# Optimization experiments

Hardware: AMD Instinct MI355X
Metric: run time of the kernel (lower is better)

## Reference

```python
import jax, jax.numpy as jnp
import numpy as np

N = 4096          # number of agents
TOP_K = 12        # config.TOP_K
OBS_RADIUS = 1.0  # config.OBS_RADIUS


def setup_inputs() -> dict:
    key = jax.random.key(0)
    ks = jax.random.split(key, 10)

    def lin(k, o, i):
        return jax.random.normal(k, (o, i), dtype=jnp.float32) * (1.0 / np.sqrt(i))

    x = jax.random.normal(ks[0], (N, N, 4), dtype=jnp.float32)
    r = jnp.asarray(0.25, dtype=jnp.float32)  # safety radius subtracted from d_norm
    W1 = lin(ks[1], 64, 6);   b1 = jax.random.normal(ks[2], (64,), jnp.float32) * 0.01
    W2 = lin(ks[3], 128, 64); b2 = jax.random.normal(ks[4], (128,), jnp.float32) * 0.01
    W3 = lin(ks[5], 64, 128); b3 = jax.random.normal(ks[6], (64,), jnp.float32) * 0.01
    W4 = lin(ks[7], 1, 64);   b4 = jax.random.normal(ks[8], (1,), jnp.float32) * 0.01
    return {"x": x, "r": r, "W1": W1, "b1": b1, "W2": W2, "b2": b2,
            "W3": W3, "b3": b3, "W4": W4, "b4": b4}


def reference(x, r, W1, b1, W2, b2, W3, b3, W4, b4):
    n = x.shape[0]
    # d_norm with eps added INSIDE the sum (matches torch: sum(x**2 + 1e-4))
    d_norm = jnp.sqrt(jnp.sum(x[:, :, :2] ** 2 + 0.0001, axis=2, keepdims=True))  # [n,n,1]
    eye = jnp.eye(n, dtype=x.dtype)[:, :, None]                                   # [n,n,1]
    xf = jnp.concatenate([x, eye, d_norm - r], axis=2)                            # [n,n,6]

    # remove_distant_agents: top-k nearest by 2D norm (eps 1e-6 inside sum)
    dn = jnp.sqrt(jnp.sum(xf[:, :, :2] ** 2 + 1e-06, axis=2))                     # [n,n]
    _, idx = jax.lax.top_k(-dn, TOP_K)                                            # [n,K]
    xg = jnp.take_along_axis(xf, idx[:, :, None], axis=1)                         # [n,K,6]

    dist = jnp.sqrt(jnp.sum(xg[:, :, :2] ** 2 + 0.0001, axis=2, keepdims=True))   # [n,K,1]
    mask = (dist <= OBS_RADIUS).astype(xg.dtype)

    # 1x1 Conv1d stack == per-neighbor MLP
    h = jax.nn.relu(jnp.einsum('nkc,oc->nko', xg, W1) + b1)
    h = jax.nn.relu(jnp.einsum('nkc,oc->nko', h, W2) + b2)
    h = jax.nn.relu(jnp.einsum('nkc,oc->nko', h, W3) + b3)
    out = (jnp.einsum('nkc,oc->nko', h, W4) + b4) * mask                          # [n,K,1]

    rows = jnp.broadcast_to(jnp.arange(n)[:, None], (n, TOP_K))
    indices = jnp.stack([rows, idx], axis=2).reshape(-1, 2)                       # [n*K,2]
    return out, mask, indices
```

## Files before the change

kernel.cpp:

```cpp
#include <hip/hip_runtime.h>

#define NN    4096
#define TOPK  12
#define NP    (NN * TOPK)
#define OFF_MASK (NP)
#define OFF_IDX  (2 * NP)

__global__ __launch_bounds__(256) void topk_rows(const float* __restrict__ x,
                                                 float* __restrict__ out) {
    const int i = blockIdx.x;
    const int t = threadIdx.x;
    const float4* x4 = (const float4*)x + (size_t)i * NN;

    float s[16];
    #pragma unroll
    for (int k = 0; k < 16; ++k) {
        float4 v = x4[(k << 8) + t];
        s[k] = v.x * v.x + v.y * v.y;
    }

    float bs = s[0];
    int   bj = t;
    #pragma unroll
    for (int k = 1; k < 16; ++k) {
        int j = (k << 8) + t;
        if (s[k] < bs) { bs = s[k]; bj = j; }
    }

    __shared__ float red_s[4];
    __shared__ int   red_j[4];
    __shared__ int   sel[TOPK];

    for (int it = 0; it < TOPK; ++it) {
        float vs = bs;
        int   vj = bj;
        #pragma unroll
        for (int off = 1; off < 64; off <<= 1) {
            float os = __shfl_xor(vs, off, 64);
            int   oj = __shfl_xor(vj, off, 64);
            if (os < vs || (os == vs && oj < vj)) { vs = os; vj = oj; }
        }
        int wid = t >> 6;
        if ((t & 63) == 0) { red_s[wid] = vs; red_j[wid] = vj; }
        __syncthreads();
        float ms = red_s[0];
        int   mj = red_j[0];
        #pragma unroll
        for (int w = 1; w < 4; ++w) {
            float osw = red_s[w]; int ojw = red_j[w];
            if (osw < ms || (osw == ms && ojw < mj)) { ms = osw; mj = ojw; }
        }
        if (t == 0) sel[it] = mj;
        if ((mj & 255) == t) {
            int kk = mj >> 8;
            #pragma unroll
            for (int k = 0; k < 16; ++k)
                if (k == kk) s[k] = 3.0e38f;
            bs = s[0]; bj = t;
            #pragma unroll
            for (int k = 1; k < 16; ++k) {
                int j = (k << 8) + t;
                if (s[k] < bs) { bs = s[k]; bj = j; }
            }
        }
        __syncthreads();
    }

    if (t < TOPK) {
        int j = sel[t];
        float4 v = x4[j];
        float ss = v.x * v.x + v.y * v.y;
        float d  = sqrtf(ss + 2.0e-4f);
        float mask = (d <= 1.0f) ? 1.0f : 0.0f;
        int p = i * TOPK + t;
        out[OFF_MASK + p]        = mask;
        out[OFF_IDX + 2 * p]     = (float)i;
        out[OFF_IDX + 2 * p + 1] = (float)j;
    }
}

__global__ __launch_bounds__(512, 6) void mlp_block(
        const float* __restrict__ x, const float* __restrict__ rp,
        const float* __restrict__ W1, const float* __restrict__ b1,
        const float* __restrict__ W2, const float* __restrict__ b2,
        const float* __restrict__ W3, const float* __restrict__ b3,
        const float* __restrict__ W4, const float* __restrict__ b4,
        float* out) {
    __shared__ float h1s[64 * 64];
    __shared__ float h2s[128 * 64];
    __shared__ float p4s[8 * 64];

    const int t  = threadIdx.x;
    const int pl = t & 63;
    const int ch = __builtin_amdgcn_readfirstlane(t >> 6);
    const int p  = blockIdx.x * 64 + pl;
    const int i  = p / TOPK;
    const int j  = (int)out[OFF_IDX + 2 * p + 1];

    const float4 v = ((const float4*)x)[(size_t)i * NN + j];
    const float d  = sqrtf(v.x * v.x + v.y * v.y + 2.0e-4f);
    float xin[6];
    xin[0] = v.x; xin[1] = v.y; xin[2] = v.z; xin[3] = v.w;
    xin[4] = (i == j) ? 1.0f : 0.0f;
    xin[5] = d - rp[0];

    #pragma unroll
    for (int q = 0; q < 8; ++q) {
        int m = ch * 8 + q;
        const float* w = W1 + m * 6;
        float a = b1[m];
        #pragma unroll
        for (int c = 0; c < 6; ++c) a += w[c] * xin[c];
        h1s[m * 64 + pl] = fmaxf(a, 0.0f);
    }
    __syncthreads();

    float acc[16];
    #pragma unroll
    for (int q = 0; q < 16; ++q) acc[q] = b2[ch * 16 + q];
    for (int part = 0; part < 4; ++part) {
        float h1r[16];
        #pragma unroll
        for (int k = 0; k < 16; ++k) h1r[k] = h1s[(part * 16 + k) * 64 + pl];
        #pragma unroll
        for (int q = 0; q < 16; ++q) {
            const float* w = W2 + (ch * 16 + q) * 64 + part * 16;
            #pragma unroll
            for (int k = 0; k < 16; ++k) acc[q] += w[k] * h1r[k];
        }
    }
    #pragma unroll
    for (int q = 0; q < 16; ++q) h2s[(ch * 16 + q) * 64 + pl] = fmaxf(acc[q], 0.0f);
    __syncthreads();

    float h3[8];
    #pragma unroll
    for (int q = 0; q < 8; ++q) h3[q] = b3[ch * 8 + q];
    for (int part = 0; part < 8; ++part) {
        float h2r[16];
        #pragma unroll
        for (int k = 0; k < 16; ++k) h2r[k] = h2s[(part * 16 + k) * 64 + pl];
        #pragma unroll
        for (int q = 0; q < 8; ++q) {
            const float* w = W3 + (ch * 8 + q) * 128 + part * 16;
            #pragma unroll
            for (int k = 0; k < 16; ++k) h3[q] += w[k] * h2r[k];
        }
    }
    float partial = 0.0f;
    #pragma unroll
    for (int q = 0; q < 8; ++q) partial += W4[ch * 8 + q] * fmaxf(h3[q], 0.0f);
    p4s[ch * 64 + pl] = partial;
    __syncthreads();

    if (t < 64) {
        float s = b4[0];
        #pragma unroll
        for (int c = 0; c < 8; ++c) s += p4s[c * 64 + t];
        int pp = blockIdx.x * 64 + t;
        out[pp] = s * out[OFF_MASK + pp];
    }
}

extern "C" void kernel_launch(void* const* d_in, const int* in_sizes, int n_in,
                              void* d_out, int out_size, void* d_ws, size_t ws_size,
                              hipStream_t stream) {
    const float* x  = (const float*)d_in[0];
    const float* rp = (const float*)d_in[1];
    const float* W1 = (const float*)d_in[2];
    const float* b1 = (const float*)d_in[3];
    const float* W2 = (const float*)d_in[4];
    const float* b2 = (const float*)d_in[5];
    const float* W3 = (const float*)d_in[6];
    const float* b3 = (const float*)d_in[7];
    const float* W4 = (const float*)d_in[8];
    const float* b4 = (const float*)d_in[9];
    float* out = (float*)d_out;

    topk_rows<<<NN, 256, 0, stream>>>(x, out);
    mlp_block<<<NP / 64, 512, 0, stream>>>(x, rp, W1, b1, W2, b2, W3, b3, W4, b4, out);
}
```

Measured before the change: 418.2 us.

## Replace block-wide top-k reduction with per-wave top-k and bitonic merge

Each wave now independently selects its own 12 smallest candidates using packed 64-bit (distance, index) keys, so each iteration needs one 64-bit shuffle reduction instead of two 32-bit ones. This removes the two block barriers per iteration. A single final bitonic sort over the 48 wave candidates picks the global top-12. The mask is computed from the stored squared distance instead of reloading x. Launch bounds add an occupancy hint. Ties are resolved by index order, which stays correct because non-negative float bits compare the same way as unsigned integers.

```diff
diff --git a/kernel.cpp b/kernel.cpp
--- a/kernel.cpp
+++ b/kernel.cpp
@@ -6,10 +6,12 @@
 #define OFF_MASK (NP)
 #define OFF_IDX  (2 * NP)
 
-__global__ __launch_bounds__(256) void topk_rows(const float* __restrict__ x,
-                                                 float* __restrict__ out) {
-    const int i = blockIdx.x;
-    const int t = threadIdx.x;
+__global__ __launch_bounds__(256, 6) void topk_rows(const float* __restrict__ x,
+                                                    float* __restrict__ out) {
+    const int i    = blockIdx.x;
+    const int t    = threadIdx.x;
+    const int lane = t & 63;
+    const int w    = t >> 6;
     const float4* x4 = (const float4*)x + (size_t)i * NN;
 
     float s[16];
@@ -19,63 +21,71 @@
         s[k] = v.x * v.x + v.y * v.y;
     }
 
-    float bs = s[0];
-    int   bj = t;
-    #pragma unroll
-    for (int k = 1; k < 16; ++k) {
-        int j = (k << 8) + t;
-        if (s[k] < bs) { bs = s[k]; bj = j; }
+    unsigned long long bk;
+    {
+        float bs = s[0]; int bj = t;
+        #pragma unroll
+        for (int k = 1; k < 16; ++k) {
+            int j = (k << 8) + t;
+            if (s[k] < bs) { bs = s[k]; bj = j; }
+        }
+        bk = ((unsigned long long)__float_as_uint(bs) << 32) | (unsigned)bj;
     }
 
-    __shared__ float red_s[4];
-    __shared__ int   red_j[4];
-    __shared__ int   sel[TOPK];
+    __shared__ unsigned long long cand[4 * TOPK];
+
+    unsigned long long mykey = ~0ULL;
 
     for (int it = 0; it < TOPK; ++it) {
-        float vs = bs;
-        int   vj = bj;
+        unsigned long long vk = bk;
         #pragma unroll
         for (int off = 1; off < 64; off <<= 1) {
-            float os = __shfl_xor(vs, off, 64);
-            int   oj = __shfl_xor(vj, off, 64);
-            if (os < vs || (os == vs && oj < vj)) { vs = os; vj = oj; }
+            unsigned long long ok = __shfl_xor(vk, off, 64);
+            vk = (ok < vk) ? ok : vk;
         }
-        int wid = t >> 6;
-        if ((t & 63) == 0) { red_s[wid] = vs; red_j[wid] = vj; }
-        __syncthreads();
-        float ms = red_s[0];
-        int   mj = red_j[0];
-        #pragma unroll
-        for (int w = 1; w < 4; ++w) {
-            float osw = red_s[w]; int ojw = red_j[w];
-            if (osw < ms || (osw == ms && ojw < mj)) { ms = osw; mj = ojw; }
-        }
-        if (t == 0) sel[it] = mj;
-        if ((mj & 255) == t) {
-            int kk = mj >> 8;
+        if (lane == it) mykey = vk;
+        int wj = (int)(vk & 0xffffffffULL);
+        if ((wj & 63) == lane) {
+            int kk = wj >> 8;
             #pragma unroll
             for (int k = 0; k < 16; ++k)
                 if (k == kk) s[k] = 3.0e38f;
-            bs = s[0]; bj = t;
+            float bs = s[0]; int bj = t;
             #pragma unroll
             for (int k = 1; k < 16; ++k) {
                 int j = (k << 8) + t;
                 if (s[k] < bs) { bs = s[k]; bj = j; }
             }
+            bk = ((unsigned long long)__float_as_uint(bs) << 32) | (unsigned)bj;
         }
-        __syncthreads();
     }
 
-    if (t < TOPK) {
-        int j = sel[t];
-        float4 v = x4[j];
-        float ss = v.x * v.x + v.y * v.y;
-        float d  = sqrtf(ss + 2.0e-4f);
-        float mask = (d <= 1.0f) ? 1.0f : 0.0f;
-        int p = i * TOPK + t;
-        out[OFF_MASK + p]        = mask;
-        out[OFF_IDX + 2 * p]     = (float)i;
-        out[OFF_IDX + 2 * p + 1] = (float)j;
+    if (lane < TOPK) cand[w * TOPK + lane] = mykey;
+    __syncthreads();
+
+    if (w == 0) {
+        unsigned long long key = (lane < 4 * TOPK) ? cand[lane] : ~0ULL;
+        #pragma unroll
+        for (int k = 2; k <= 64; k <<= 1) {
+            #pragma unroll
+            for (int jj = k >> 1; jj >= 1; jj >>= 1) {
+                unsigned long long ok = __shfl_xor(key, jj, 64);
+                bool keepMin = ((lane & k) == 0) == ((lane & jj) == 0);
+                unsigned long long mn = (ok < key) ? ok : key;
+                unsigned long long mx = (ok < key) ? key : ok;
+                key = keepMin ? mn : mx;
+            }
+        }
+        if (lane < TOPK) {
+            int   j  = (int)(key & 0xffffffffULL);
+            float ss = __uint_as_float((unsigned)(key >> 32));
+            float d  = sqrtf(ss + 2.0e-4f);
+            float mask = (d <= 1.0f) ? 1.0f : 0.0f;
+            int p = i * TOPK + lane;
+            out[OFF_MASK + p]        = mask;
+            out[OFF_IDX + 2 * p]     = (float)i;
+            out[OFF_IDX + 2 * p + 1] = (float)j;
+        }
     }
 }
 
```

Measured after the change: 412.5 us. Within noise of the previous version (-1.4%).
